# Kernel optimization log

Hardware: AMD Instinct MI355X
Metric: run time of the kernel (lower is better)

## Reference

```python
import jax, jax.numpy as jnp
import numpy as np

L, H, DH = 2, 4, 64
D = H * DH                      # hidden_dim*heads = 256
B = 8                           # graphs per batch
NI_PG, ND_PG = 1024, 512        # inst/data nodes per graph
NI, ND = B * NI_PG, B * ND_PG
NPG = NI_PG + ND_PG
KPOOL = NPG // 2                # SAGPooling ratio=0.5
EC, EI, EO, EK = 65536, 32768, 32768, 8192


def setup_inputs():
    key = jax.random.key(0)
    ks = iter(jax.random.split(key, 64))
    def edges(ns, nd, e):
        k1, k2 = jax.random.split(next(ks))
        return jnp.stack([jax.random.randint(k1, (e,), 0, ns),
                          jax.random.randint(k2, (e,), 0, nd)]).astype(jnp.int32)
    inp = {}
    for g in ('g1', 'g2'):
        inp[g + '_x_inst'] = 0.1 * jax.random.normal(next(ks), (NI, D), jnp.float32)
        inp[g + '_x_data'] = 0.1 * jax.random.normal(next(ks), (ND, D), jnp.float32)
        inp[g + '_e_control'] = edges(NI, NI, EC)
        inp[g + '_e_input'] = edges(ND, NI, EI)
        inp[g + '_e_output'] = edges(NI, ND, EO)
        inp[g + '_e_call'] = edges(NI, NI, EK)
    s = 1.0 / np.sqrt(D)
    def w(*shape):
        return s * jax.random.normal(next(ks), shape, jnp.float32)
    for name in ('hgt_Wk', 'hgt_Wq', 'hgt_Wv', 'hgt_Wo'):
        inp[name] = w(L, 2, 2, D, D)   # [layer, direction, node_type, D, D]
    sh = 1.0 / np.sqrt(DH)
    inp['hgt_arel'] = sh * jax.random.normal(next(ks), (L, 2, 4, H, DH, DH), jnp.float32)
    inp['hgt_mrel'] = sh * jax.random.normal(next(ks), (L, 2, 4, H, DH, DH), jnp.float32)
    inp['hgt_prel'] = jnp.ones((L, 2, 4, H), jnp.float32)
    inp['hgt_skip'] = jnp.ones((L, 2, 2), jnp.float32)
    inp['pool_W'] = w(D, 1)
    inp['pool_att'] = 0.1 * jax.random.normal(next(ks), (2,), jnp.float32)
    inp['pool_bias'] = jnp.zeros((1,), jnp.float32)
    for name in ('trans_Wq', 'trans_Wk', 'trans_Wv', 'trans_Wo'):
        inp[name] = w(D, D)
    inp['trans_ln_g'] = jnp.ones((D,), jnp.float32)
    inp['trans_ln_b'] = jnp.zeros((D,), jnp.float32)
    return inp


def _seg_softmax_agg(scores, vals, col, n):
    # scores [E,H], vals [E,H,DH], softmax over incoming edges per dst node
    m = jax.ops.segment_max(scores, col, num_segments=n)
    a = jnp.exp(scores - m[col])
    den = jax.ops.segment_sum(a, col, num_segments=n)
    alpha = a / (den[col] + 1e-16)
    return jax.ops.segment_sum(alpha[..., None] * vals, col, num_segments=n)


def _hgt_conv(xs, rels, Wk, Wq, Wv, Wo, arel, mrel, prel, skip):
    # xs: [x_inst, x_data]; rels: list of (rel_idx, src_t, dst_t, row, col)
    ns = [x.shape[0] for x in xs]
    K = [(x @ Wk[t]).reshape(-1, H, DH) for t, x in enumerate(xs)]
    Q = [(x @ Wq[t]).reshape(-1, H, DH) for t, x in enumerate(xs)]
    V = [(x @ Wv[t]).reshape(-1, H, DH) for t, x in enumerate(xs)]
    buf = {0: ([], [], []), 1: ([], [], [])}
    for r, st, dt, row, col in rels:
        ke = jnp.einsum('ehd,hdf->ehf', K[st][row], arel[r])
        ve = jnp.einsum('ehd,hdf->ehf', V[st][row], mrel[r])
        sc = (Q[dt][col] * ke).sum(-1) * prel[r] / np.sqrt(DH)   # [E,H]
        buf[dt][0].append(sc); buf[dt][1].append(ve); buf[dt][2].append(col)
    out = []
    for t, x in enumerate(xs):
        sc = jnp.concatenate(buf[t][0])
        ve = jnp.concatenate(buf[t][1])
        col = jnp.concatenate(buf[t][2])
        agg = _seg_softmax_agg(sc, ve, col, ns[t]).reshape(ns[t], D)
        o = jax.nn.gelu(agg, approximate=False) @ Wo[t]
        g = jax.nn.sigmoid(skip[t])
        out.append(g * o + (1.0 - g) * x)
    return out


def _dir_hgt(xs, E, P, l):
    (rc, cc), (ri, ci), (ro, co), (rk, ck) = [(e[0], e[1]) for e in E]
    fwd_rels = [(0, 0, 0, rc, cc), (1, 1, 0, ri, ci), (2, 0, 1, ro, co), (3, 0, 0, rk, ck)]
    rev_rels = [(0, 0, 0, cc, rc), (1, 0, 1, ci, ri), (2, 1, 0, co, ro), (3, 0, 0, ck, rk)]
    of = _hgt_conv(xs, fwd_rels, *[p[l, 0] for p in P])
    orv = _hgt_conv(xs, rev_rels, *[p[l, 1] for p in P])
    return [0.5 * a + 0.5 * b for a, b in zip(of, orv)]   # alpha = 0.5


def _branch(x_i, x_d, ec, ei, eo, ek, P, pool_W, pool_att, pool_bias, tq, tk, tv, to, lg, lb):
    xs = [x_i, x_d]
    E = (ec, ei, eo, ek)
    for l in range(L):
        xs = _dir_hgt(xs, E, P, l)
        xs = [jax.nn.relu(x) for x in xs]        # dropout is identity at eval
    x = jnp.concatenate(xs, 0)                   # to_homogeneous: inst then data
    N = NI + ND
    loops = jnp.arange(N, dtype=jnp.int32)       # GATConv add_self_loops=True
    row = jnp.concatenate([ec[0], ei[0] + NI, eo[0], ek[0], loops])
    col = jnp.concatenate([ec[1], ei[1], eo[1] + NI, ek[1], loops])
    # SAGPooling score via 1-channel GATConv
    h = x @ pool_W                               # [N,1]
    e = jax.nn.leaky_relu(pool_att[0] * h[row, 0] + pool_att[1] * h[col, 0], negative_slope=0.2)
    m = jax.ops.segment_max(e, col, num_segments=N)
    a = jnp.exp(e - m[col])
    den = jax.ops.segment_sum(a, col, num_segments=N)
    score = jax.ops.segment_sum((a / (den[col] + 1e-16)) * h[row, 0], col, num_segments=N) + pool_bias[0]
    # regroup nodes per graph (graphs contiguous within each node type block)
    sg = jnp.concatenate([score[:NI].reshape(B, NI_PG), score[NI:].reshape(B, ND_PG)], 1)
    xg = jnp.concatenate([x[:NI].reshape(B, NI_PG, D), x[NI:].reshape(B, ND_PG, D)], 1)
    vals, idx = jax.lax.top_k(sg, KPOOL)
    xp = jnp.take_along_axis(xg, idx[:, :, None], axis=1) * jnp.tanh(vals)[:, :, None]
    # global transformer attention over pooled nodes of each graph (TransConv)
    q = (xp @ tq).reshape(B, KPOOL, H, DH)
    k_ = (xp @ tk).reshape(B, KPOOL, H, DH)
    v = (xp @ tv).reshape(B, KPOOL, H, DH)
    att = jax.nn.softmax(jnp.einsum('bqhd,bkhd->bhqk', q, k_) / np.sqrt(DH), -1)
    o = jnp.einsum('bhqk,bkhd->bqhd', att, v).reshape(B, KPOOL, D) @ to
    y = xp + o
    mu = y.mean(-1, keepdims=True)
    var = ((y - mu) ** 2).mean(-1, keepdims=True)
    gatt = lg * (y - mu) / jnp.sqrt(var + 1e-5) + lb
    feat = jnp.concatenate([xp, gatt], -1)       # [B, KPOOL, 2D]
    return feat.sum(1)                           # global_add_pool -> [B, 2D]


def reference(g1_x_inst, g1_x_data, g1_e_control, g1_e_input, g1_e_output, g1_e_call,
              g2_x_inst, g2_x_data, g2_e_control, g2_e_input, g2_e_output, g2_e_call,
              hgt_Wk, hgt_Wq, hgt_Wv, hgt_Wo, hgt_arel, hgt_mrel, hgt_prel, hgt_skip,
              pool_W, pool_att, pool_bias,
              trans_Wq, trans_Wk, trans_Wv, trans_Wo, trans_ln_g, trans_ln_b):
    P = (hgt_Wk, hgt_Wq, hgt_Wv, hgt_Wo, hgt_arel, hgt_mrel, hgt_prel, hgt_skip)
    u = _branch(g1_x_inst, g1_x_data, g1_e_control, g1_e_input, g1_e_output, g1_e_call,
                P, pool_W, pool_att, pool_bias, trans_Wq, trans_Wk, trans_Wv, trans_Wo,
                trans_ln_g, trans_ln_b)
    v = _branch(g2_x_inst, g2_x_data, g2_e_control, g2_e_input, g2_e_output, g2_e_call,
                P, pool_W, pool_att, pool_bias, trans_Wq, trans_Wk, trans_Wv, trans_Wo,
                trans_ln_g, trans_ln_b)
    num = (u * v).sum(-1)
    den = jnp.maximum(jnp.linalg.norm(u, axis=-1), 1e-8) * jnp.maximum(jnp.linalg.norm(v, axis=-1), 1e-8)
    return num / den                             # cosine similarity, [B]
```

## Files before the change

### kernel.cpp

```cpp
#include <hip/hip_runtime.h>
#include <math.h>
#include <stdint.h>

#define LL 2
#define HH 4
#define DHH 64
#define DD 256
#define BB 8
#define NI 8192
#define ND 4096
#define NROW 12288
#define KPOOL 768
#define EC 65536
#define EI 32768
#define EO 32768
#define EK 8192
#define EHGT (EC+EI+EO+EK)

typedef unsigned short u16;
typedef short bf16x8 __attribute__((ext_vector_type(8)));
typedef float f32x4 __attribute__((ext_vector_type(4)));
typedef unsigned short u16x4 __attribute__((ext_vector_type(4)));

__device__ inline float gelu_f(float x){ return 0.5f*x*(1.f+erff(x*0.70710678118654752f)); }
__device__ inline u16 f2b(float x){ uint32_t u=__float_as_uint(x); return (u16)((u + 0x7fffu + ((u>>16)&1u))>>16); }
__device__ inline float b2f(u16 h){ return __uint_as_float(((uint32_t)h)<<16); }

__global__ void fill_u32(uint32_t* p, uint32_t v, int n){
    int i = blockIdx.x*256 + threadIdx.x;
    if(i<n) p[i]=v;
}

__global__ void cvt_split(const float* __restrict__ A, int nA, const float* __restrict__ B, int nB,
                          u16* __restrict__ oh, u16* __restrict__ ol){
    int i = (blockIdx.x*256 + threadIdx.x)*4;
    int tot = nA + nB;
    if(i >= tot) return;
    float4 v = (i < nA) ? *(const float4*)(A + i) : *(const float4*)(B + (i - nA));
    float vv[4] = {v.x, v.y, v.z, v.w};
    u16x4 h4, l4;
    #pragma unroll
    for(int j=0;j<4;j++){
        float x = vv[j];
        u16 h = f2b(x);
        h4[j] = h;
        l4[j] = f2b(x - b2f(h));
    }
    *(u16x4*)(oh + i) = h4;
    *(u16x4*)(ol + i) = l4;
}

struct WCArgs { const float* in[8]; u16* oh[8]; u16* ol[8]; int cnt[8]; int nr; };
__global__ void wcvt_split(WCArgs a){
    int mat = blockIdx.y, ri = 0;
    while(ri < a.nr-1 && mat >= a.cnt[ri]){ mat -= a.cnt[ri]; ri++; }
    const float* in = a.in[ri] + (size_t)mat*65536;
    u16* oh = a.oh[ri] + (size_t)mat*65536;
    u16* ol = a.ol[ri] + (size_t)mat*65536;
    int n = blockIdx.x, k = threadIdx.x;
    float x = in[(size_t)k*DD + n];
    u16 h = f2b(x);
    oh[n*DD + k] = h;
    ol[n*DD + k] = f2b(x - b2f(h));
}

struct GDesc { const u16* Ah; const u16* Al; const u16* Bh; const u16* Bl;
               float* C; u16* Oh; u16* Ol;
               const float* X; float* Xacc; const float* skipp;
               int mblks; int mode; int prec; };
struct GArgs { GDesc d[20]; int nd; };

__global__ __launch_bounds__(256) void gemm_mfma(GArgs ga){
    __shared__ u16 SBUF[2*128*64];
    char* Abuf = (char*)SBUF;
    char* Bbuf = (char*)(SBUF + 128*64);
    int mb = blockIdx.x, di = 0;
    while(di < ga.nd-1 && mb >= ga.d[di].mblks){ mb -= ga.d[di].mblks; di++; }
    GDesc g = ga.d[di];
    const int prec = g.prec;
    const int m0 = mb*128, n0 = blockIdx.y*128;
    const int tid = threadIdx.x;
    const int lane = tid & 63, wid = tid >> 6;
    const int wm = (wid>>1)*64, wn = (wid&1)*64;
    const int l15 = lane & 15, l4 = lane >> 4;
    const int srow = tid >> 1, hf = tid & 1;
    const int ssw = (srow&7)<<4;
    const int c0 = (hf*32) ^ ssw;
    const int c1 = (hf*32+16) ^ ssw;
    const int c2 = (64+hf*32) ^ ssw;
    const int c3 = (64+hf*32+16) ^ ssw;
    const int rbyte = srow*128;
    const u16* __restrict__ Aph = g.Ah + (size_t)(m0 + srow)*DD + hf*16;
    const u16* __restrict__ Apl = g.Al + (size_t)(m0 + srow)*DD + hf*16;
    const u16* __restrict__ Bph = g.Bh + (size_t)(n0 + srow)*DD + hf*16;
    const u16* __restrict__ Bpl = g.Bl + (size_t)(n0 + srow)*DD + hf*16;
    f32x4 acc[4][4] = {};
    bf16x8 r0, r1, r2, r3, r4, r5, r6, r7;
    r0 = *(const bf16x8*)(Aph);
    r1 = *(const bf16x8*)(Aph + 8);
    r4 = *(const bf16x8*)(Bph);
    r5 = *(const bf16x8*)(Bph + 8);
    if(!prec){
        r2 = *(const bf16x8*)(Apl);
        r3 = *(const bf16x8*)(Apl + 8);
        r6 = *(const bf16x8*)(Bpl);
        r7 = *(const bf16x8*)(Bpl + 8);
    }
    #pragma unroll
    for(int k0=0;k0<DD;k0+=32){
        __syncthreads();
        *(bf16x8*)(Abuf + rbyte + c0) = r0; *(bf16x8*)(Abuf + rbyte + c1) = r1;
        *(bf16x8*)(Bbuf + rbyte + c0) = r4; *(bf16x8*)(Bbuf + rbyte + c1) = r5;
        if(!prec){
            *(bf16x8*)(Abuf + rbyte + c2) = r2; *(bf16x8*)(Abuf + rbyte + c3) = r3;
            *(bf16x8*)(Bbuf + rbyte + c2) = r6; *(bf16x8*)(Bbuf + rbyte + c3) = r7;
        }
        __syncthreads();
        if(k0 + 32 < DD){
            int kn = k0 + 32;
            r0 = *(const bf16x8*)(Aph + kn);     r1 = *(const bf16x8*)(Aph + kn + 8);
            r4 = *(const bf16x8*)(Bph + kn);     r5 = *(const bf16x8*)(Bph + kn + 8);
            if(!prec){
                r2 = *(const bf16x8*)(Apl + kn); r3 = *(const bf16x8*)(Apl + kn + 8);
                r6 = *(const bf16x8*)(Bpl + kn); r7 = *(const bf16x8*)(Bpl + kn + 8);
            }
        }
        bf16x8 afh[4], bfh[4];
        #pragma unroll
        for(int i=0;i<4;i++){
            int ar = wm + i*16 + l15;
            int abase = ar*128;
            afh[i] = *(const bf16x8*)(Abuf + abase + ((l4*16) ^ ((ar&7)<<4)));
            int br = wn + i*16 + l15;
            int bbase = br*128;
            bfh[i] = *(const bf16x8*)(Bbuf + bbase + ((l4*16) ^ ((br&7)<<4)));
        }
        #pragma unroll
        for(int i=0;i<4;i++)
            #pragma unroll
            for(int j=0;j<4;j++)
                acc[i][j] = __builtin_amdgcn_mfma_f32_16x16x32_bf16(afh[i], bfh[j], acc[i][j], 0,0,0);
        if(!prec){
            bf16x8 afl[4], bfl[4];
            #pragma unroll
            for(int i=0;i<4;i++){
                int ar = wm + i*16 + l15;
                int abase = ar*128;
                afl[i] = *(const bf16x8*)(Abuf + abase + ((64 + l4*16) ^ ((ar&7)<<4)));
                int br = wn + i*16 + l15;
                int bbase = br*128;
                bfl[i] = *(const bf16x8*)(Bbuf + bbase + ((64 + l4*16) ^ ((br&7)<<4)));
            }
            #pragma unroll
            for(int i=0;i<4;i++)
                #pragma unroll
                for(int j=0;j<4;j++){
                    acc[i][j] = __builtin_amdgcn_mfma_f32_16x16x32_bf16(afh[i], bfl[j], acc[i][j], 0,0,0);
                    acc[i][j] = __builtin_amdgcn_mfma_f32_16x16x32_bf16(afl[i], bfh[j], acc[i][j], 0,0,0);
                }
        }
    }
    const int mode = g.mode;
    float gg = 0.f;
    if(mode == 2 || mode == 3) gg = 1.f/(1.f + expf(-*g.skipp));
    float* LDSf = (float*)SBUF;
    const int lrow = tid >> 5;
    const int cc4 = (tid & 31)*4;
    #pragma unroll
    for(int half=0; half<2; half++){
        __syncthreads();
        if((wid>>1) == half){
            #pragma unroll
            for(int i=0;i<4;i++)
                #pragma unroll
                for(int j=0;j<4;j++)
                    #pragma unroll
                    for(int r=0;r<4;r++)
                        LDSf[(i*16 + l4*4 + r)*128 + wn + j*16 + l15] = acc[i][j][r];
        }
        __syncthreads();
        #pragma unroll
        for(int k=0;k<8;k++){
            int row = lrow + k*8;
            size_t o = (size_t)(m0 + half*64 + row)*DD + n0 + cc4;
            float4 v = *(const float4*)&LDSf[row*128 + cc4];
            float vv[4] = {v.x, v.y, v.z, v.w};
            if(mode==0){
                *(float4*)(g.C + o) = v;
            } else if(mode==4){
                u16x4 h4;
                #pragma unroll
                for(int j=0;j<4;j++) h4[j] = f2b(vv[j]);
                *(u16x4*)(g.Oh + o) = h4;
            } else if(mode==1){
                u16x4 h4, lo4;
                #pragma unroll
                for(int j=0;j<4;j++){
                    u16 hh = f2b(vv[j]); h4[j]=hh; lo4[j]=f2b(vv[j]-b2f(hh));
                }
                *(u16x4*)(g.Oh + o) = h4;
                *(u16x4*)(g.Ol + o) = lo4;
            } else if(mode==2){
                float4 x = *(const float4*)(g.X + o);
                float xx[4] = {x.x, x.y, x.z, x.w};
                float4 w;
                float* ww = (float*)&w;
                #pragma unroll
                for(int j=0;j<4;j++) ww[j] = 0.5f*(gg*vv[j] + (1.f-gg)*xx[j]);
                *(float4*)(g.Xacc + o) = w;
            } else {
                float4 x = *(const float4*)(g.X + o);
                float4 xa = *(const float4*)(g.Xacc + o);
                float xx[4] = {x.x, x.y, x.z, x.w};
                float aa[4] = {xa.x, xa.y, xa.z, xa.w};
                float4 cv;
                float* cvv = (float*)&cv;
                u16x4 h4, lo4;
                #pragma unroll
                for(int j=0;j<4;j++){
                    float v3 = aa[j] + 0.5f*(gg*vv[j] + (1.f-gg)*xx[j]);
                    v3 = v3 > 0.f ? v3 : 0.f;
                    cvv[j] = v3;
                    u16 hh = f2b(v3); h4[j]=hh; lo4[j]=f2b(v3-b2f(hh));
                }
                *(float4*)(g.C + o) = cv;
                *(u16x4*)(g.Oh + o) = h4;
                *(u16x4*)(g.Ol + o) = lo4;
            }
        }
    }
}

__global__ void combine_all(const float* __restrict__ Wk, const float* __restrict__ Wv,
                            const float* __restrict__ Ra, const float* __restrict__ Rm,
                            float* __restrict__ wtk, float* __restrict__ wtv){
    const int st_tab[2][4] = {{0,1,0,0},{0,0,1,0}};
    int combo = blockIdx.y;
    int idx = combo >> 1, kv = combo & 1;
    int r = idx & 3, wb = idx >> 2, dir = wb & 1;
    int st = st_tab[dir][r];
    const float* W = (kv ? Wv : Wk) + (size_t)(wb*2 + st)*65536;
    const float* R = (kv ? Rm : Ra) + (size_t)idx*16384;
    float* o = (kv ? wtv : wtk) + (size_t)idx*65536;
    int d = blockIdx.x, c = threadIdx.x;
    int h = c >> 6, f = c & 63;
    const float* Wrow = W + d*DD + h*64;
    const float* Rh = R + h*4096 + f;
    float s = 0.f;
    #pragma unroll 8
    for(int k=0;k<64;k++) s += Wrow[k]*Rh[k*64];
    o[d*DD + c] = s;
}

__device__ inline void edge_decode(int e, int& r, int& el){
    if(e < EC){ r=0; el=e; }
    else if(e < EC+EI){ r=1; el=e-EC; }
    else if(e < EC+EI+EO){ r=2; el=e-(EC+EI); }
    else { r=3; el=e-(EC+EI+EO); }
}

struct CB2 {
    const int* row[8]; const int* col[8];
    int dt[8]; int st[8];
    uint32_t* cnt; uint32_t* rowptr; uint32_t* einfo;
};

__global__ void csr_hist2(CB2 a){
    int ge = blockIdx.x*256 + threadIdx.x;
    if(ge >= 2*EHGT) return;
    int dir = ge >= EHGT;
    int e = ge - dir*EHGT;
    int r, el; edge_decode(e, r, el);
    int idx = dir*4 + r;
    int c = a.col[idx][el];
    int dst = dir*NROW + (a.dt[idx] ? (NI + c) : c);
    atomicAdd(&a.cnt[dst], 1u);
}

__global__ __launch_bounds__(1024) void scan_rowptr2(uint32_t* cnt, uint32_t* rowptr){
    __shared__ uint32_t part[1024];
    int t = threadIdx.x;
    int base = t*24;
    uint32_t lpre[24];
    uint32_t sum = 0;
    #pragma unroll
    for(int i=0;i<24;i++){
        uint32_t c = cnt[base+i];
        lpre[i] = sum; sum += c;
        cnt[base+i] = 0;
    }
    part[t] = sum;
    __syncthreads();
    for(int offs=1; offs<1024; offs<<=1){
        uint32_t v = (t>=offs) ? part[t-offs] : 0u;
        __syncthreads();
        part[t] += v;
        __syncthreads();
    }
    uint32_t pre = (t==0) ? 0u : part[t-1];
    #pragma unroll
    for(int i=0;i<24;i++) rowptr[base+i] = pre + lpre[i];
    if(t==1023) rowptr[2*NROW] = part[1023];
}

__global__ void csr_scatter2(CB2 a){
    int ge = blockIdx.x*256 + threadIdx.x;
    if(ge >= 2*EHGT) return;
    int dir = ge >= EHGT;
    int e = ge - dir*EHGT;
    int r, el; edge_decode(e, r, el);
    int idx = dir*4 + r;
    int c = a.col[idx][el];
    int dst = dir*NROW + (a.dt[idx] ? (NI + c) : c);
    int src = a.row[idx][el];
    uint32_t p = a.rowptr[dst] + atomicAdd(&a.cnt[dst], 1u);
    uint32_t vmidx = (uint32_t)(r*NI + src);
    uint32_t hom = a.st[idx] ? (uint32_t)(NI + src) : (uint32_t)src;
    a.einfo[p] = vmidx | (hom << 16);
}

__global__ __launch_bounds__(256) void hgt_fused(const uint32_t* __restrict__ rowptr,
                                                 const uint32_t* __restrict__ einfo,
                                                 const float* __restrict__ q_i,
                                                 const float* __restrict__ q_d,
                                                 const u16* __restrict__ ka,
                                                 const u16* __restrict__ vm,
                                                 const float* __restrict__ prel,
                                                 u16* __restrict__ bagg_h,
                                                 u16* __restrict__ bagg_l){
    int wv = threadIdx.x >> 6, lane = threadIdx.x & 63;
    int rowi = blockIdx.x*4 + wv;
    uint32_t p0 = rowptr[rowi], p1 = rowptr[rowi+1];
    int h = lane >> 4;
    const float* qrow = (rowi < NI) ? (q_i + (size_t)rowi*DD) : (q_d + (size_t)(rowi-NI)*DD);
    float4 q4 = *(const float4*)(qrow + lane*4);
    float pr0 = prel[0*HH+h]*0.125f, pr1 = prel[1*HH+h]*0.125f;
    float pr2 = prel[2*HH+h]*0.125f, pr3 = prel[3*HH+h]*0.125f;
    float m = -INFINITY, den = 0.f;
    float4 o4 = {0.f,0.f,0.f,0.f};
    for(uint32_t p = p0; p < p1; p++){
        uint32_t vmidx = einfo[p] & 0xffffu;
        int r = vmidx >> 13;
        uint2 kr = *(const uint2*)(ka + (size_t)vmidx*DD + lane*4);
        uint2 vr = *(const uint2*)(vm + (size_t)vmidx*DD + lane*4);
        float k0 = __uint_as_float(kr.x << 16), k1 = __uint_as_float(kr.x & 0xffff0000u);
        float k2 = __uint_as_float(kr.y << 16), k3 = __uint_as_float(kr.y & 0xffff0000u);
        float v0 = __uint_as_float(vr.x << 16), v1 = __uint_as_float(vr.x & 0xffff0000u);
        float v2 = __uint_as_float(vr.y << 16), v3 = __uint_as_float(vr.y & 0xffff0000u);
        float d = q4.x*k0 + q4.y*k1 + q4.z*k2 + q4.w*k3;
        d += __shfl_xor(d, 1); d += __shfl_xor(d, 2);
        d += __shfl_xor(d, 4); d += __shfl_xor(d, 8);
        float pf = (r==0) ? pr0 : (r==1) ? pr1 : (r==2) ? pr2 : pr3;
        float s = d * pf;
        float nm = fmaxf(m, s);
        float sc_ = expf(m - nm);
        float pe = expf(s - nm);
        den = den*sc_ + pe;
        o4.x = o4.x*sc_ + pe*v0;
        o4.y = o4.y*sc_ + pe*v1;
        o4.z = o4.z*sc_ + pe*v2;
        o4.w = o4.w*sc_ + pe*v3;
        m = nm;
    }
    float inv = 1.f/(den + 1e-16f);
    float vals[4] = {o4.x*inv, o4.y*inv, o4.z*inv, o4.w*inv};
    u16x4 h4, l4;
    #pragma unroll
    for(int j=0;j<4;j++){
        float g = gelu_f(vals[j]);
        u16 hh = f2b(g);
        h4[j] = hh;
        l4[j] = f2b(g - b2f(hh));
    }
    size_t ob = (size_t)rowi*DD + lane*4;
    *(u16x4*)(bagg_h + ob) = h4;
    *(u16x4*)(bagg_l + ob) = l4;
}

__global__ void pool_h2(const float* __restrict__ xi, const float* __restrict__ xd,
                        const float* __restrict__ w, float* __restrict__ h){
    int node = blockIdx.x*4 + (threadIdx.x>>6);
    int lane = threadIdx.x & 63;
    const float* xr = (node < NI) ? (xi + (size_t)node*DD) : (xd + (size_t)(node-NI)*DD);
    float s = 0.f;
    for(int j=lane;j<DD;j+=64) s += xr[j]*w[j];
    for(int m=32;m;m>>=1) s += __shfl_xor(s, m);
    if(lane==0) h[node] = s;
}

__global__ __launch_bounds__(256) void pool_csr(const uint32_t* __restrict__ rowptr,
                                                const uint32_t* __restrict__ einfo,
                                                const float* __restrict__ h,
                                                const float* __restrict__ att,
                                                float* __restrict__ score){
    int w = blockIdx.x*4 + (threadIdx.x >> 6);
    int lane = threadIdx.x & 63;
    if(w >= NROW) return;
    uint32_t p0 = rowptr[w], p1 = rowptr[w+1];
    float a0 = att[0], a1 = att[1];
    float hn = h[w];
    float es = a0*hn + a1*hn;
    es = es >= 0.f ? es : 0.2f*es;
    float m = -INFINITY;
    for(uint32_t p = p0+lane; p < p1; p += 64){
        float hs = h[einfo[p] >> 16];
        float e = a0*hs + a1*hn;
        e = e >= 0.f ? e : 0.2f*e;
        m = fmaxf(m, e);
    }
    #pragma unroll
    for(int s=32;s;s>>=1) m = fmaxf(m, __shfl_xor(m, s));
    m = fmaxf(m, es);
    float lden = 0.f, lnum = 0.f;
    for(uint32_t p = p0+lane; p < p1; p += 64){
        float hs = h[einfo[p] >> 16];
        float e = a0*hs + a1*hn;
        e = e >= 0.f ? e : 0.2f*e;
        float a = expf(e - m);
        lden += a; lnum += a*hs;
    }
    #pragma unroll
    for(int s=32;s;s>>=1){ lden += __shfl_xor(lden, s); lnum += __shfl_xor(lnum, s); }
    float aself = expf(es - m);
    lden += aself; lnum += aself*hn;
    if(lane==0) score[w] = lnum/(lden + 1e-16f);
}

__global__ __launch_bounds__(256) void topk_rank(const float* __restrict__ score,
                                                 const float* __restrict__ bias,
                                                 int* __restrict__ sel_node,
                                                 float* __restrict__ sel_scale){
    int b = blockIdx.y;
    int wid = threadIdx.x >> 6, lane = threadIdx.x & 63;
    int i = blockIdx.x*4 + wid;
    int nodei = (i<1024) ? (b*1024 + i) : (NI + b*512 + (i-1024));
    float ki = score[nodei];
    int r = 0;
    #pragma unroll
    for(int s=0;s<24;s++){
        int j = s*64 + lane;
        int nodej = (j<1024) ? (b*1024 + j) : (NI + b*512 + (j-1024));
        float kj = score[nodej];
        r += (kj > ki) || (kj == ki && j < i);
    }
    #pragma unroll
    for(int m=32;m;m>>=1) r += __shfl_xor(r, m);
    if(lane==0 && r < KPOOL){
        sel_node[b*KPOOL + r] = nodei;
        sel_scale[b*KPOOL + r] = tanhf(ki + bias[0]);
    }
}

__global__ void gather_xp(const int* __restrict__ sel, const float* __restrict__ scale,
                          const float* __restrict__ xi, const float* __restrict__ xd,
                          float* __restrict__ xp, u16* __restrict__ bh, u16* __restrict__ bl){
    int i = blockIdx.x*256 + threadIdx.x;
    int rowp = i >> 8, c = i & 255;
    int node = sel[rowp];
    float s = scale[rowp];
    float v = (node < NI) ? xi[(size_t)node*DD + c] : xd[(size_t)(node-NI)*DD + c];
    float x = v*s;
    xp[i] = x;
    u16 hh = f2b(x);
    bh[i] = hh;
    bl[i] = f2b(x - b2f(hh));
}

__global__ __launch_bounds__(256) void attn_mfma(const u16* __restrict__ Qh,
                                                 const u16* __restrict__ Kh,
                                                 const u16* __restrict__ Vh,
                                                 u16* __restrict__ aoh, u16* __restrict__ aol){
    __shared__ u16 KhS[64*64], VtS[64*64];
    char* KhB = (char*)KhS; char* VtB = (char*)VtS;
    int bh = blockIdx.x;
    int b = bh >> 2, h = bh & 3;
    int q0 = blockIdx.y * 64;
    int tid = threadIdx.x;
    int lane = tid & 63;
    int w = tid >> 6;
    int l15 = lane & 15, l4 = lane >> 4;
    size_t qrow = (size_t)(b*KPOOL + q0 + w*16 + l15);
    bf16x8 qh[2];
    #pragma unroll
    for(int c=0;c<2;c++)
        qh[c] = *(const bf16x8*)(Qh + qrow*DD + h*64 + c*32 + l4*8);
    float mreg = -INFINITY, lreg = 0.f;
    f32x4 O[4] = {};
    for(int k0=0;k0<KPOOL;k0+=64){
        __syncthreads();
        {
            int row = tid >> 2, q4 = tid & 3;
            size_t gbase = ((size_t)(b*KPOOL + k0 + row))*DD + h*64 + q4*16;
            bf16x8 k0v = *(const bf16x8*)(Kh + gbase);
            bf16x8 k1v = *(const bf16x8*)(Kh + gbase + 8);
            int sw = (row&7)<<4;
            int colb = q4*32;
            *(bf16x8*)(KhB + row*128 + (colb ^ sw))      = k0v;
            *(bf16x8*)(KhB + row*128 + ((colb+16) ^ sw)) = k1v;
            int row0 = (tid >> 3)*2, dhg = (tid & 7)*8;
            size_t vbase = ((size_t)(b*KPOOL + k0 + row0))*DD + h*64 + dhg;
            bf16x8 va = *(const bf16x8*)(Vh + vbase);
            bf16x8 vb = *(const bf16x8*)(Vh + vbase + DD);
            #pragma unroll
            for(int j=0;j<8;j++){
                int dh = dhg + j;
                uint32_t pk = (uint32_t)(u16)(short)va[j] | ((uint32_t)(u16)(short)vb[j] << 16);
                *(uint32_t*)(VtB + dh*128 + ((row0*2) ^ ((dh&7)<<4))) = pk;
            }
        }
        __syncthreads();
        f32x4 s[4] = {};
        #pragma unroll
        for(int t=0;t<4;t++){
            int arow = t*16 + l15;
            int sw = (arow&7)<<4;
            const char* bh_ = KhB + arow*128;
            bf16x8 kh0 = *(const bf16x8*)(bh_ + ((l4*16) ^ sw));
            bf16x8 kh1 = *(const bf16x8*)(bh_ + ((l4*16 + 64) ^ sw));
            s[t] = __builtin_amdgcn_mfma_f32_16x16x32_bf16(kh0, qh[0], s[t], 0,0,0);
            s[t] = __builtin_amdgcn_mfma_f32_16x16x32_bf16(kh1, qh[1], s[t], 0,0,0);
        }
        float cm = -INFINITY;
        #pragma unroll
        for(int t=0;t<4;t++)
            #pragma unroll
            for(int r=0;r<4;r++){ s[t][r] *= 0.125f; cm = fmaxf(cm, s[t][r]); }
        cm = fmaxf(cm, __shfl_xor(cm,16));
        cm = fmaxf(cm, __shfl_xor(cm,32));
        float nm = fmaxf(mreg, cm);
        float es = expf(mreg - nm);
        float ps = 0.f;
        #pragma unroll
        for(int t=0;t<4;t++)
            #pragma unroll
            for(int r=0;r<4;r++){ float pv = expf(s[t][r] - nm); s[t][r] = pv; ps += pv; }
        ps += __shfl_xor(ps,16);
        ps += __shfl_xor(ps,32);
        lreg = lreg*es + ps;
        mreg = nm;
        #pragma unroll
        for(int d=0;d<4;d++){ O[d][0]*=es; O[d][1]*=es; O[d][2]*=es; O[d][3]*=es; }
        #pragma unroll
        for(int c32=0;c32<2;c32++){
            bf16x8 pb;
            #pragma unroll
            for(int j=0;j<8;j++){
                int srcl = ((((lane>>4)*2 + (j>>2)) & 3) << 4) | l15;
                float v0 = __shfl(s[c32*2+0][j&3], srcl, 64);
                float v1 = __shfl(s[c32*2+1][j&3], srcl, 64);
                float v = (lane < 32) ? v0 : v1;
                pb[j] = (short)f2b(v);
            }
            #pragma unroll
            for(int dhb=0; dhb<4; dhb++){
                int vrow = dhb*16 + l15;
                bf16x8 va = *(const bf16x8*)(VtB + vrow*128 + ((c32*64 + l4*16) ^ ((vrow&7)<<4)));
                O[dhb] = __builtin_amdgcn_mfma_f32_16x16x32_bf16(va, pb, O[dhb], 0,0,0);
            }
        }
    }
    float inv = 1.f/lreg;
    #pragma unroll
    for(int dhb=0;dhb<4;dhb++)
        #pragma unroll
        for(int r=0;r<4;r++){
            float val = O[dhb][r]*inv;
            size_t o = qrow*DD + h*64 + dhb*16 + l4*4 + r;
            u16 hh = f2b(val);
            aoh[o] = hh;
            aol[o] = f2b(val - b2f(hh));
        }
}

__global__ __launch_bounds__(256) void ln_kernel(const float* __restrict__ xp, const float* __restrict__ o2,
                                                 const float* __restrict__ lg, const float* __restrict__ lb,
                                                 float* __restrict__ gatt){
    __shared__ float red[256];
    int r = blockIdx.x, c = threadIdx.x;
    float y = xp[(size_t)r*DD + c] + o2[(size_t)r*DD + c];
    red[c] = y; __syncthreads();
    for(int s=128;s;s>>=1){ if(c<s) red[c] += red[c+s]; __syncthreads(); }
    float mu = red[0]*(1.f/DD);
    __syncthreads();
    float d = y - mu;
    red[c] = d*d; __syncthreads();
    for(int s=128;s;s>>=1){ if(c<s) red[c] += red[c+s]; __syncthreads(); }
    float var = red[0]*(1.f/DD);
    gatt[(size_t)r*DD + c] = lg[c]*d/sqrtf(var+1e-5f) + lb[c];
}

__global__ void feat_reduce2(const float* __restrict__ xp, const float* __restrict__ gatt,
                             float* __restrict__ out){
    int b = blockIdx.x, c = threadIdx.x;
    int j0 = blockIdx.y*64;
    float s1=0.f, s2=0.f;
    for(int j=j0;j<j0+64;j++){
        size_t base = ((size_t)(b*KPOOL + j))*DD + c;
        s1 += xp[base];
        s2 += gatt[base];
    }
    atomicAdd(&out[b*512 + c], s1);
    atomicAdd(&out[b*512 + 256 + c], s2);
}

__global__ void cosine_kernel(const float* __restrict__ u, const float* __restrict__ v,
                              float* __restrict__ out){
    int b = blockIdx.x, t = threadIdx.x;
    float du=0.f, nu=0.f, nv=0.f;
    for(int j=t;j<512;j+=64){
        float a = u[b*512+j], bb = v[b*512+j];
        du += a*bb; nu += a*a; nv += bb*bb;
    }
    for(int m=32;m;m>>=1){
        du += __shfl_xor(du,m); nu += __shfl_xor(nu,m); nv += __shfl_xor(nv,m);
    }
    if(t==0) out[b] = du / (fmaxf(sqrtf(nu),1e-8f)*fmaxf(sqrtf(nv),1e-8f));
}

extern "C" void kernel_launch(void* const* d_in, const int* in_sizes, int n_in,
                              void* d_out, int out_size, void* d_ws, size_t ws_size,
                              hipStream_t stream){
    (void)in_sizes; (void)n_in; (void)out_size; (void)ws_size;
    const float* hgt_Wk   = (const float*)d_in[12];
    const float* hgt_Wq   = (const float*)d_in[13];
    const float* hgt_Wv   = (const float*)d_in[14];
    const float* hgt_Wo   = (const float*)d_in[15];
    const float* hgt_arel = (const float*)d_in[16];
    const float* hgt_mrel = (const float*)d_in[17];
    const float* hgt_prel = (const float*)d_in[18];
    const float* hgt_skip = (const float*)d_in[19];
    const float* pool_W   = (const float*)d_in[20];
    const float* pool_att = (const float*)d_in[21];
    const float* pool_bias= (const float*)d_in[22];
    const float* t_wq     = (const float*)d_in[23];
    const float* t_wk     = (const float*)d_in[24];
    const float* t_wv     = (const float*)d_in[25];
    const float* t_wo     = (const float*)d_in[26];
    const float* ln_g     = (const float*)d_in[27];
    const float* ln_b     = (const float*)d_in[28];
    float* out = (float*)d_out;

    char* base = (char*)d_ws;
    size_t off = 0;
    auto allocb = [&](size_t nbytes)->void*{
        void* p = (void*)(base + off);
        off += ((nbytes + 255) & ~(size_t)255);
        return p;
    };
    const size_t MAT = 65536;
    u16* bwtk_h = (u16*)allocb(16*MAT*2); u16* bwtk_l = (u16*)allocb(16*MAT*2);
    u16* bwtv_h = (u16*)allocb(16*MAT*2); u16* bwtv_l = (u16*)allocb(16*MAT*2);
    u16* bwq_h  = (u16*)allocb(8*MAT*2);  u16* bwq_l  = (u16*)allocb(8*MAT*2);
    u16* bwo_h  = (u16*)allocb(8*MAT*2);  u16* bwo_l  = (u16*)allocb(8*MAT*2);
    u16* btw_h  = (u16*)allocb(4*MAT*2);  u16* btw_l  = (u16*)allocb(4*MAT*2);
    float* ubuf = (float*)allocb(BB*512*4);
    float* vbuf = (float*)allocb(BB*512*4);
    float* xa_i = (float*)allocb((size_t)NI*DD*4);
    float* xa_d = (float*)allocb((size_t)ND*DD*4);
    float* xb_i = (float*)allocb((size_t)NI*DD*4);
    float* xb_d = (float*)allocb((size_t)ND*DD*4);
    uint32_t* ccnt   = (uint32_t*)allocb((size_t)2*NROW*4);
    uint32_t* rowptr = (uint32_t*)allocb((size_t)(2*NROW+1)*4);
    uint32_t* einfo  = (uint32_t*)allocb((size_t)2*EHGT*4);
    size_t region = off;
    float* q_i  = (float*)allocb((size_t)2*NI*DD*4);
    float* q_d  = (float*)allocb((size_t)2*ND*DD*4);
    u16* ka16 = (u16*)allocb((size_t)8*NI*DD*2);
    u16* vm16 = (u16*)allocb((size_t)8*NI*DD*2);
    float* xacc_i= (float*)allocb((size_t)NI*DD*4);
    float* xacc_d= (float*)allocb((size_t)ND*DD*4);
    u16* bcur_h = (u16*)allocb((size_t)NROW*DD*2);
    u16* bcur_l = (u16*)allocb((size_t)NROW*DD*2);
    u16* bagg_h = (u16*)allocb((size_t)NROW*DD*2);
    u16* bagg_l = (u16*)allocb((size_t)NROW*DD*2);
    off = region;
    float* hvec = (float*)allocb(NROW*4);
    float* pscore = (float*)allocb(NROW*4);
    int* seln   = (int*)allocb(BB*KPOOL*4);
    float* sels = (float*)allocb(BB*KPOOL*4);
    float* xp   = (float*)allocb((size_t)BB*KPOOL*DD*4);
    float* o2   = (float*)allocb((size_t)BB*KPOOL*DD*4);
    float* gatt = (float*)allocb((size_t)BB*KPOOL*DD*4);
    u16* bxp_h = (u16*)allocb((size_t)BB*KPOOL*DD*2);
    u16* bxp_l = (u16*)allocb((size_t)BB*KPOOL*DD*2);
    u16* qbh = (u16*)allocb((size_t)BB*KPOOL*DD*2);
    u16* kbh = (u16*)allocb((size_t)BB*KPOOL*DD*2);
    u16* vbh = (u16*)allocb((size_t)BB*KPOOL*DD*2);
    u16* bao_h = (u16*)allocb((size_t)BB*KPOOL*DD*2);
    u16* bao_l = (u16*)allocb((size_t)BB*KPOOL*DD*2);

    const int st_tab[2][4] = {{0,1,0,0},{0,0,1,0}};
    const int dt_tab[2][4] = {{0,0,1,0},{0,1,0,0}};
    const int MR = BB*KPOOL;

    fill_u32<<<(2*BB*512+255)/256,256,0,stream>>>((uint32_t*)ubuf, 0u, 2*BB*512);
    float* wtkF = (float*)ka16;
    float* wtvF = (float*)ka16 + 16*MAT;
    combine_all<<<dim3(256,32),256,0,stream>>>(hgt_Wk, hgt_Wv, hgt_arel, hgt_mrel, wtkF, wtvF);
    WCArgs wc;
    wc.in[0]=wtkF;   wc.oh[0]=bwtk_h; wc.ol[0]=bwtk_l; wc.cnt[0]=16;
    wc.in[1]=wtvF;   wc.oh[1]=bwtv_h; wc.ol[1]=bwtv_l; wc.cnt[1]=16;
    wc.in[2]=hgt_Wq; wc.oh[2]=bwq_h;  wc.ol[2]=bwq_l;  wc.cnt[2]=8;
    wc.in[3]=hgt_Wo; wc.oh[3]=bwo_h;  wc.ol[3]=bwo_l;  wc.cnt[3]=8;
    wc.in[4]=t_wq;   wc.oh[4]=btw_h;          wc.ol[4]=btw_l;          wc.cnt[4]=1;
    wc.in[5]=t_wk;   wc.oh[5]=btw_h+1*MAT;    wc.ol[5]=btw_l+1*MAT;    wc.cnt[5]=1;
    wc.in[6]=t_wv;   wc.oh[6]=btw_h+2*MAT;    wc.ol[6]=btw_l+2*MAT;    wc.cnt[6]=1;
    wc.in[7]=t_wo;   wc.oh[7]=btw_h+3*MAT;    wc.ol[7]=btw_l+3*MAT;    wc.cnt[7]=1;
    wc.nr = 8;
    wcvt_split<<<dim3(256,52),256,0,stream>>>(wc);

    for(int bi=0;bi<2;bi++){
        int ib = bi*6;
        const float* x_inst = (const float*)d_in[ib+0];
        const float* x_data = (const float*)d_in[ib+1];
        const int* ecp = (const int*)d_in[ib+2];
        const int* eip = (const int*)d_in[ib+3];
        const int* eop = (const int*)d_in[ib+4];
        const int* ekp = (const int*)d_in[ib+5];
        const int* rows_f[4] = {ecp, eip, eop, ekp};
        const int* cols_f[4] = {ecp+EC, eip+EI, eop+EO, ekp+EK};

        CB2 cb;
        for(int r=0;r<4;r++){
            cb.row[r]   = rows_f[r]; cb.col[r]   = cols_f[r]; cb.dt[r]   = dt_tab[0][r]; cb.st[r]   = st_tab[0][r];
            cb.row[4+r] = cols_f[r]; cb.col[4+r] = rows_f[r]; cb.dt[4+r] = dt_tab[1][r]; cb.st[4+r] = st_tab[1][r];
        }
        cb.cnt = ccnt; cb.rowptr = rowptr; cb.einfo = einfo;
        fill_u32<<<(2*NROW+255)/256,256,0,stream>>>(ccnt, 0u, 2*NROW);
        csr_hist2<<<(2*EHGT+255)/256,256,0,stream>>>(cb);
        scan_rowptr2<<<1,1024,0,stream>>>(ccnt, rowptr);
        csr_scatter2<<<(2*EHGT+255)/256,256,0,stream>>>(cb);

        const float* cur_i = x_inst;
        const float* cur_d = x_data;
        cvt_split<<<((NROW*DD/4)+255)/256,256,0,stream>>>(cur_i, NI*DD, cur_d, ND*DD, bcur_h, bcur_l);
        for(int l=0;l<LL;l++){
            float* nxt_i = (l==0) ? xa_i : xb_i;
            float* nxt_d = (l==0) ? xa_d : xb_d;

            GArgs g1; int nb1 = 0, ndx = 0;
            auto addg = [&](int srctype, const u16* Bh, const u16* Bl, float* Cm, u16* Om, int M, int mode, int prec){
                GDesc& d = g1.d[ndx];
                size_t ao = srctype ? (size_t)NI*DD : 0;
                d.Ah = bcur_h + ao; d.Al = bcur_l + ao;
                d.Bh = Bh; d.Bl = Bl; d.C = Cm;
                d.Oh = Om; d.Ol = nullptr; d.X = nullptr; d.Xacc = nullptr; d.skipp = nullptr;
                d.mblks = M/128; d.mode = mode; d.prec = prec;
                nb1 += M/128; ndx++;
            };
            for(int dir=0;dir<2;dir++){
                int wb = l*2 + dir;
                addg(0, bwq_h + (size_t)(wb*2+0)*MAT, bwq_l + (size_t)(wb*2+0)*MAT,
                     q_i + (size_t)dir*NI*DD, nullptr, NI, 0, 0);
                addg(1, bwq_h + (size_t)(wb*2+1)*MAT, bwq_l + (size_t)(wb*2+1)*MAT,
                     q_d + (size_t)dir*ND*DD, nullptr, ND, 0, 0);
                for(int r=0;r<4;r++){
                    int st = st_tab[dir][r];
                    addg(st, bwtk_h + (size_t)(wb*4+r)*MAT, bwtk_l + (size_t)(wb*4+r)*MAT,
                         nullptr, ka16 + (size_t)(dir*4 + r)*NI*DD, st ? ND : NI, 4, 1);
                }
                for(int r=0;r<4;r++){
                    int st = st_tab[dir][r];
                    addg(st, bwtv_h + (size_t)(wb*4+r)*MAT, bwtv_l + (size_t)(wb*4+r)*MAT,
                         nullptr, vm16 + (size_t)(dir*4 + r)*NI*DD, st ? ND : NI, 4, 1);
                }
            }
            g1.nd = ndx;
            gemm_mfma<<<dim3(nb1,2),256,0,stream>>>(g1);

            for(int dir=0;dir<2;dir++){
                int wb = l*2 + dir;

                hgt_fused<<<NROW/4,256,0,stream>>>(rowptr + (size_t)dir*NROW, einfo,
                    q_i + (size_t)dir*NI*DD, q_d + (size_t)dir*ND*DD,
                    ka16 + (size_t)dir*4*NI*DD, vm16 + (size_t)dir*4*NI*DD,
                    hgt_prel + (size_t)wb*4*HH, bagg_h, bagg_l);

                GArgs g3; g3.nd = 2;
                for(int t=0;t<2;t++){
                    GDesc& d = g3.d[t];
                    size_t ao = t ? (size_t)NI*DD : 0;
                    d.Ah = bagg_h + ao; d.Al = bagg_l + ao;
                    d.Bh = bwo_h + (size_t)(wb*2+t)*MAT; d.Bl = bwo_l + (size_t)(wb*2+t)*MAT;
                    d.C = t ? nxt_d : nxt_i;
                    d.Oh = bcur_h + ao; d.Ol = bcur_l + ao;
                    d.X = t ? cur_d : cur_i;
                    d.Xacc = t ? xacc_d : xacc_i;
                    d.skipp = hgt_skip + wb*2 + t;
                    d.mblks = (t ? ND : NI)/128;
                    d.mode = dir ? 3 : 2;
                    d.prec = 0;
                }
                gemm_mfma<<<dim3(NI/128 + ND/128,2),256,0,stream>>>(g3);
            }
            cur_i = nxt_i;
            cur_d = nxt_d;
        }

        pool_h2<<<NROW/4,256,0,stream>>>(cur_i, cur_d, pool_W, hvec);
        pool_csr<<<NROW/4,256,0,stream>>>(rowptr, einfo, hvec, pool_att, pscore);
        topk_rank<<<dim3(384,BB),256,0,stream>>>(pscore, pool_bias, seln, sels);
        gather_xp<<<BB*KPOOL,256,0,stream>>>(seln, sels, cur_i, cur_d, xp, bxp_h, bxp_l);

        GArgs g4; g4.nd = 3;
        for(int t=0;t<3;t++){
            GDesc& d = g4.d[t];
            d.Ah=bxp_h; d.Al=bxp_l;
            d.Bh=btw_h + (size_t)t*MAT; d.Bl=btw_l + (size_t)t*MAT;
            d.C = nullptr;
            d.Oh = (t==0)? qbh : (t==1)? kbh : vbh;
            d.Ol = nullptr;
            d.X = nullptr; d.Xacc = nullptr; d.skipp = nullptr;
            d.mblks = MR/128; d.mode = 4; d.prec = 0;
        }
        gemm_mfma<<<dim3(3*(MR/128),2),256,0,stream>>>(g4);
        attn_mfma<<<dim3(BB*HH, KPOOL/64),256,0,stream>>>(qbh, kbh, vbh, bao_h, bao_l);
        GArgs g5; g5.nd = 1;
        {
            GDesc& d = g5.d[0];
            d.Ah=bao_h; d.Al=bao_l;
            d.Bh=btw_h + (size_t)3*MAT; d.Bl=btw_l + (size_t)3*MAT;
            d.C=o2; d.Oh=nullptr; d.Ol=nullptr; d.X=nullptr; d.Xacc=nullptr; d.skipp=nullptr;
            d.mblks=MR/128; d.mode=0; d.prec=0;
        }
        gemm_mfma<<<dim3(MR/128,2),256,0,stream>>>(g5);
        ln_kernel<<<MR,256,0,stream>>>(xp, o2, ln_g, ln_b, gatt);
        feat_reduce2<<<dim3(BB,12),256,0,stream>>>(xp, gatt, bi ? vbuf : ubuf);
    }

    cosine_kernel<<<BB,64,0,stream>>>(ubuf, vbuf, out);
}
```

Before: 951.0 us.

## Merge both HGT directions into one K=512 output GEMM with prescaled weights

Both edge directions of the HGT aggregation now run in one hgt_fused launch that writes a concatenated [row, 512] aggregate. One output-projection GEMM with K=512 then consumes it, using Wo weights prescaled by 0.5*sigmoid(skip) and stacked along K. The skip and residual terms collapse into a single coefficient on X, which removes the Xacc intermediate buffer, one extra GEMM launch and one hgt launch per layer. In exchange, the GEMM K loop is no longer fully unrolled because K is now a runtime value, and the aggregate buffer doubles in size.

```diff
diff --git a/kernel.cpp b/kernel.cpp
--- a/kernel.cpp
+++ b/kernel.cpp
@@ -64,10 +64,27 @@
     ol[n*DD + k] = f2b(x - b2f(h));
 }
 
+__global__ void wcvt_wo(const float* __restrict__ Wo, const float* __restrict__ skip,
+                        u16* __restrict__ oh, u16* __restrict__ ol){
+    int combo = blockIdx.y;
+    int l = combo >> 1, t = combo & 1;
+    int n = blockIdx.x, k = threadIdx.x;
+    #pragma unroll
+    for(int dir=0;dir<2;dir++){
+        int wi = (l*2+dir)*2 + t;
+        float gg = 1.f/(1.f+expf(-skip[wi]));
+        float x = 0.5f*gg*Wo[(size_t)wi*65536 + (size_t)k*DD + n];
+        size_t o = (size_t)combo*131072 + (size_t)n*512 + dir*256 + k;
+        u16 hh = f2b(x);
+        oh[o] = hh;
+        ol[o] = f2b(x - b2f(hh));
+    }
+}
+
 struct GDesc { const u16* Ah; const u16* Al; const u16* Bh; const u16* Bl;
                float* C; u16* Oh; u16* Ol;
-               const float* X; float* Xacc; const float* skipp;
-               int mblks; int mode; int prec; };
+               const float* X; const float* skipp;
+               int mblks; int mode; int prec; int kdim; };
 struct GArgs { GDesc d[20]; int nd; };
 
 __global__ __launch_bounds__(256) void gemm_mfma(GArgs ga){
@@ -78,6 +95,7 @@
     while(di < ga.nd-1 && mb >= ga.d[di].mblks){ mb -= ga.d[di].mblks; di++; }
     GDesc g = ga.d[di];
     const int prec = g.prec;
+    const int KD = g.kdim;
     const int m0 = mb*128, n0 = blockIdx.y*128;
     const int tid = threadIdx.x;
     const int lane = tid & 63, wid = tid >> 6;
@@ -90,10 +108,10 @@
     const int c2 = (64+hf*32) ^ ssw;
     const int c3 = (64+hf*32+16) ^ ssw;
     const int rbyte = srow*128;
-    const u16* __restrict__ Aph = g.Ah + (size_t)(m0 + srow)*DD + hf*16;
-    const u16* __restrict__ Apl = g.Al + (size_t)(m0 + srow)*DD + hf*16;
-    const u16* __restrict__ Bph = g.Bh + (size_t)(n0 + srow)*DD + hf*16;
-    const u16* __restrict__ Bpl = g.Bl + (size_t)(n0 + srow)*DD + hf*16;
+    const u16* __restrict__ Aph = g.Ah + (size_t)(m0 + srow)*KD + hf*16;
+    const u16* __restrict__ Apl = g.Al + (size_t)(m0 + srow)*KD + hf*16;
+    const u16* __restrict__ Bph = g.Bh + (size_t)(n0 + srow)*KD + hf*16;
+    const u16* __restrict__ Bpl = g.Bl + (size_t)(n0 + srow)*KD + hf*16;
     f32x4 acc[4][4] = {};
     bf16x8 r0, r1, r2, r3, r4, r5, r6, r7;
     r0 = *(const bf16x8*)(Aph);
@@ -106,8 +124,7 @@
         r6 = *(const bf16x8*)(Bpl);
         r7 = *(const bf16x8*)(Bpl + 8);
     }
-    #pragma unroll
-    for(int k0=0;k0<DD;k0+=32){
+    for(int k0=0;k0<KD;k0+=32){
         __syncthreads();
         *(bf16x8*)(Abuf + rbyte + c0) = r0; *(bf16x8*)(Abuf + rbyte + c1) = r1;
         *(bf16x8*)(Bbuf + rbyte + c0) = r4; *(bf16x8*)(Bbuf + rbyte + c1) = r5;
@@ -116,7 +133,7 @@
             *(bf16x8*)(Bbuf + rbyte + c2) = r6; *(bf16x8*)(Bbuf + rbyte + c3) = r7;
         }
         __syncthreads();
-        if(k0 + 32 < DD){
+        if(k0 + 32 < KD){
             int kn = k0 + 32;
             r0 = *(const bf16x8*)(Aph + kn);     r1 = *(const bf16x8*)(Aph + kn + 8);
             r4 = *(const bf16x8*)(Bph + kn);     r5 = *(const bf16x8*)(Bph + kn + 8);
@@ -161,8 +178,12 @@
         }
     }
     const int mode = g.mode;
-    float gg = 0.f;
-    if(mode == 2 || mode == 3) gg = 1.f/(1.f + expf(-*g.skipp));
+    float cx = 0.f;
+    if(mode == 6){
+        float g0 = 1.f/(1.f + expf(-g.skipp[0]));
+        float g1 = 1.f/(1.f + expf(-g.skipp[2]));
+        cx = 1.f - 0.5f*(g0 + g1);
+    }
     float* LDSf = (float*)SBUF;
     const int lrow = tid >> 5;
     const int cc4 = (tid & 31)*4;
@@ -192,33 +213,15 @@
                 #pragma unroll
                 for(int j=0;j<4;j++) h4[j] = f2b(vv[j]);
                 *(u16x4*)(g.Oh + o) = h4;
-            } else if(mode==1){
-                u16x4 h4, lo4;
-                #pragma unroll
-                for(int j=0;j<4;j++){
-                    u16 hh = f2b(vv[j]); h4[j]=hh; lo4[j]=f2b(vv[j]-b2f(hh));
-                }
-                *(u16x4*)(g.Oh + o) = h4;
-                *(u16x4*)(g.Ol + o) = lo4;
-            } else if(mode==2){
+            } else {
                 float4 x = *(const float4*)(g.X + o);
                 float xx[4] = {x.x, x.y, x.z, x.w};
-                float4 w;
-                float* ww = (float*)&w;
-                #pragma unroll
-                for(int j=0;j<4;j++) ww[j] = 0.5f*(gg*vv[j] + (1.f-gg)*xx[j]);
-                *(float4*)(g.Xacc + o) = w;
-            } else {
-                float4 x = *(const float4*)(g.X + o);
-                float4 xa = *(const float4*)(g.Xacc + o);
-                float xx[4] = {x.x, x.y, x.z, x.w};
-                float aa[4] = {xa.x, xa.y, xa.z, xa.w};
                 float4 cv;
                 float* cvv = (float*)&cv;
                 u16x4 h4, lo4;
                 #pragma unroll
                 for(int j=0;j<4;j++){
-                    float v3 = aa[j] + 0.5f*(gg*vv[j] + (1.f-gg)*xx[j]);
+                    float v3 = vv[j] + cx*xx[j];
                     v3 = v3 > 0.f ? v3 : 0.f;
                     cvv[j] = v3;
                     u16 hh = f2b(v3); h4[j]=hh; lo4[j]=f2b(v3-b2f(hh));
@@ -329,20 +332,28 @@
                                                  u16* __restrict__ bagg_h,
                                                  u16* __restrict__ bagg_l){
     int wv = threadIdx.x >> 6, lane = threadIdx.x & 63;
-    int rowi = blockIdx.x*4 + wv;
-    uint32_t p0 = rowptr[rowi], p1 = rowptr[rowi+1];
+    int bx = blockIdx.x;
+    int dir = bx >= (NROW/4);
+    bx -= dir*(NROW/4);
+    int rowi = bx*4 + wv;
+    uint32_t p0 = rowptr[(size_t)dir*NROW + rowi], p1 = rowptr[(size_t)dir*NROW + rowi + 1];
     int h = lane >> 4;
-    const float* qrow = (rowi < NI) ? (q_i + (size_t)rowi*DD) : (q_d + (size_t)(rowi-NI)*DD);
+    const float* qi = q_i + (size_t)dir*NI*DD;
+    const float* qd = q_d + (size_t)dir*ND*DD;
+    const u16* kad = ka + (size_t)dir*4*NI*DD;
+    const u16* vmd = vm + (size_t)dir*4*NI*DD;
+    const float* pr = prel + dir*4*HH;
+    const float* qrow = (rowi < NI) ? (qi + (size_t)rowi*DD) : (qd + (size_t)(rowi-NI)*DD);
     float4 q4 = *(const float4*)(qrow + lane*4);
-    float pr0 = prel[0*HH+h]*0.125f, pr1 = prel[1*HH+h]*0.125f;
-    float pr2 = prel[2*HH+h]*0.125f, pr3 = prel[3*HH+h]*0.125f;
+    float pr0 = pr[0*HH+h]*0.125f, pr1 = pr[1*HH+h]*0.125f;
+    float pr2 = pr[2*HH+h]*0.125f, pr3 = pr[3*HH+h]*0.125f;
     float m = -INFINITY, den = 0.f;
     float4 o4 = {0.f,0.f,0.f,0.f};
     for(uint32_t p = p0; p < p1; p++){
         uint32_t vmidx = einfo[p] & 0xffffu;
         int r = vmidx >> 13;
-        uint2 kr = *(const uint2*)(ka + (size_t)vmidx*DD + lane*4);
-        uint2 vr = *(const uint2*)(vm + (size_t)vmidx*DD + lane*4);
+        uint2 kr = *(const uint2*)(kad + (size_t)vmidx*DD + lane*4);
+        uint2 vr = *(const uint2*)(vmd + (size_t)vmidx*DD + lane*4);
         float k0 = __uint_as_float(kr.x << 16), k1 = __uint_as_float(kr.x & 0xffff0000u);
         float k2 = __uint_as_float(kr.y << 16), k3 = __uint_as_float(kr.y & 0xffff0000u);
         float v0 = __uint_as_float(vr.x << 16), v1 = __uint_as_float(vr.x & 0xffff0000u);
@@ -372,7 +383,7 @@
         h4[j] = hh;
         l4[j] = f2b(g - b2f(hh));
     }
-    size_t ob = (size_t)rowi*DD + lane*4;
+    size_t ob = (size_t)rowi*512 + dir*256 + lane*4;
     *(u16x4*)(bagg_h + ob) = h4;
     *(u16x4*)(bagg_l + ob) = l4;
 }
@@ -651,7 +662,7 @@
     u16* bwtk_h = (u16*)allocb(16*MAT*2); u16* bwtk_l = (u16*)allocb(16*MAT*2);
     u16* bwtv_h = (u16*)allocb(16*MAT*2); u16* bwtv_l = (u16*)allocb(16*MAT*2);
     u16* bwq_h  = (u16*)allocb(8*MAT*2);  u16* bwq_l  = (u16*)allocb(8*MAT*2);
-    u16* bwo_h  = (u16*)allocb(8*MAT*2);  u16* bwo_l  = (u16*)allocb(8*MAT*2);
+    u16* bwoc_h = (u16*)allocb(4*131072*2); u16* bwoc_l = (u16*)allocb(4*131072*2);
     u16* btw_h  = (u16*)allocb(4*MAT*2);  u16* btw_l  = (u16*)allocb(4*MAT*2);
     float* ubuf = (float*)allocb(BB*512*4);
     float* vbuf = (float*)allocb(BB*512*4);
@@ -667,12 +678,10 @@
     float* q_d  = (float*)allocb((size_t)2*ND*DD*4);
     u16* ka16 = (u16*)allocb((size_t)8*NI*DD*2);
     u16* vm16 = (u16*)allocb((size_t)8*NI*DD*2);
-    float* xacc_i= (float*)allocb((size_t)NI*DD*4);
-    float* xacc_d= (float*)allocb((size_t)ND*DD*4);
     u16* bcur_h = (u16*)allocb((size_t)NROW*DD*2);
     u16* bcur_l = (u16*)allocb((size_t)NROW*DD*2);
-    u16* bagg_h = (u16*)allocb((size_t)NROW*DD*2);
-    u16* bagg_l = (u16*)allocb((size_t)NROW*DD*2);
+    u16* bagg_h = (u16*)allocb((size_t)NROW*512*2);
+    u16* bagg_l = (u16*)allocb((size_t)NROW*512*2);
     off = region;
     float* hvec = (float*)allocb(NROW*4);
     float* pscore = (float*)allocb(NROW*4);
@@ -701,13 +710,13 @@
     wc.in[0]=wtkF;   wc.oh[0]=bwtk_h; wc.ol[0]=bwtk_l; wc.cnt[0]=16;
     wc.in[1]=wtvF;   wc.oh[1]=bwtv_h; wc.ol[1]=bwtv_l; wc.cnt[1]=16;
     wc.in[2]=hgt_Wq; wc.oh[2]=bwq_h;  wc.ol[2]=bwq_l;  wc.cnt[2]=8;
-    wc.in[3]=hgt_Wo; wc.oh[3]=bwo_h;  wc.ol[3]=bwo_l;  wc.cnt[3]=8;
-    wc.in[4]=t_wq;   wc.oh[4]=btw_h;          wc.ol[4]=btw_l;          wc.cnt[4]=1;
-    wc.in[5]=t_wk;   wc.oh[5]=btw_h+1*MAT;    wc.ol[5]=btw_l+1*MAT;    wc.cnt[5]=1;
-    wc.in[6]=t_wv;   wc.oh[6]=btw_h+2*MAT;    wc.ol[6]=btw_l+2*MAT;    wc.cnt[6]=1;
-    wc.in[7]=t_wo;   wc.oh[7]=btw_h+3*MAT;    wc.ol[7]=btw_l+3*MAT;    wc.cnt[7]=1;
-    wc.nr = 8;
-    wcvt_split<<<dim3(256,52),256,0,stream>>>(wc);
+    wc.in[3]=t_wq;   wc.oh[3]=btw_h;          wc.ol[3]=btw_l;          wc.cnt[3]=1;
+    wc.in[4]=t_wk;   wc.oh[4]=btw_h+1*MAT;    wc.ol[4]=btw_l+1*MAT;    wc.cnt[4]=1;
+    wc.in[5]=t_wv;   wc.oh[5]=btw_h+2*MAT;    wc.ol[5]=btw_l+2*MAT;    wc.cnt[5]=1;
+    wc.in[6]=t_wo;   wc.oh[6]=btw_h+3*MAT;    wc.ol[6]=btw_l+3*MAT;    wc.cnt[6]=1;
+    wc.nr = 7;
+    wcvt_split<<<dim3(256,44),256,0,stream>>>(wc);
+    wcvt_wo<<<dim3(256,4),256,0,stream>>>(hgt_Wo, hgt_skip, bwoc_h, bwoc_l);
 
     for(int bi=0;bi<2;bi++){
         int ib = bi*6;
@@ -744,8 +753,8 @@
                 size_t ao = srctype ? (size_t)NI*DD : 0;
                 d.Ah = bcur_h + ao; d.Al = bcur_l + ao;
                 d.Bh = Bh; d.Bl = Bl; d.C = Cm;
-                d.Oh = Om; d.Ol = nullptr; d.X = nullptr; d.Xacc = nullptr; d.skipp = nullptr;
-                d.mblks = M/128; d.mode = mode; d.prec = prec;
+                d.Oh = Om; d.Ol = nullptr; d.X = nullptr; d.skipp = nullptr;
+                d.mblks = M/128; d.mode = mode; d.prec = prec; d.kdim = 256;
                 nb1 += M/128; ndx++;
             };
             for(int dir=0;dir<2;dir++){
@@ -768,31 +777,26 @@
             g1.nd = ndx;
             gemm_mfma<<<dim3(nb1,2),256,0,stream>>>(g1);
 
-            for(int dir=0;dir<2;dir++){
-                int wb = l*2 + dir;
-
-                hgt_fused<<<NROW/4,256,0,stream>>>(rowptr + (size_t)dir*NROW, einfo,
-                    q_i + (size_t)dir*NI*DD, q_d + (size_t)dir*ND*DD,
-                    ka16 + (size_t)dir*4*NI*DD, vm16 + (size_t)dir*4*NI*DD,
-                    hgt_prel + (size_t)wb*4*HH, bagg_h, bagg_l);
-
-                GArgs g3; g3.nd = 2;
-                for(int t=0;t<2;t++){
-                    GDesc& d = g3.d[t];
-                    size_t ao = t ? (size_t)NI*DD : 0;
-                    d.Ah = bagg_h + ao; d.Al = bagg_l + ao;
-                    d.Bh = bwo_h + (size_t)(wb*2+t)*MAT; d.Bl = bwo_l + (size_t)(wb*2+t)*MAT;
-                    d.C = t ? nxt_d : nxt_i;
-                    d.Oh = bcur_h + ao; d.Ol = bcur_l + ao;
-                    d.X = t ? cur_d : cur_i;
-                    d.Xacc = t ? xacc_d : xacc_i;
-                    d.skipp = hgt_skip + wb*2 + t;
-                    d.mblks = (t ? ND : NI)/128;
-                    d.mode = dir ? 3 : 2;
-                    d.prec = 0;
-                }
-                gemm_mfma<<<dim3(NI/128 + ND/128,2),256,0,stream>>>(g3);
+            hgt_fused<<<2*(NROW/4),256,0,stream>>>(rowptr, einfo,
+                q_i, q_d, ka16, vm16, hgt_prel + (size_t)l*2*4*HH, bagg_h, bagg_l);
+
+            GArgs g3; g3.nd = 2;
+            for(int t=0;t<2;t++){
+                GDesc& d = g3.d[t];
+                d.Ah = bagg_h + (t ? (size_t)NI*512 : 0);
+                d.Al = bagg_l + (t ? (size_t)NI*512 : 0);
+                d.Bh = bwoc_h + (size_t)(l*2+t)*131072;
+                d.Bl = bwoc_l + (size_t)(l*2+t)*131072;
+                d.C = t ? nxt_d : nxt_i;
+                d.Oh = bcur_h + (t ? (size_t)NI*DD : 0);
+                d.Ol = bcur_l + (t ? (size_t)NI*DD : 0);
+                d.X = t ? cur_d : cur_i;
+                d.skipp = hgt_skip + l*4 + t;
+                d.mblks = (t ? ND : NI)/128;
+                d.mode = 6; d.prec = 0; d.kdim = 512;
             }
+            gemm_mfma<<<dim3(NI/128 + ND/128,2),256,0,stream>>>(g3);
+
             cur_i = nxt_i;
             cur_d = nxt_d;
         }
@@ -810,8 +814,8 @@
             d.C = nullptr;
             d.Oh = (t==0)? qbh : (t==1)? kbh : vbh;
             d.Ol = nullptr;
-            d.X = nullptr; d.Xacc = nullptr; d.skipp = nullptr;
-            d.mblks = MR/128; d.mode = 4; d.prec = 0;
+            d.X = nullptr; d.skipp = nullptr;
+            d.mblks = MR/128; d.mode = 4; d.prec = 0; d.kdim = 256;
         }
         gemm_mfma<<<dim3(3*(MR/128),2),256,0,stream>>>(g4);
         attn_mfma<<<dim3(BB*HH, KPOOL/64),256,0,stream>>>(qbh, kbh, vbh, bao_h, bao_l);
@@ -820,8 +824,8 @@
             GDesc& d = g5.d[0];
             d.Ah=bao_h; d.Al=bao_l;
             d.Bh=btw_h + (size_t)3*MAT; d.Bl=btw_l + (size_t)3*MAT;
-            d.C=o2; d.Oh=nullptr; d.Ol=nullptr; d.X=nullptr; d.Xacc=nullptr; d.skipp=nullptr;
-            d.mblks=MR/128; d.mode=0; d.prec=0;
+            d.C=o2; d.Oh=nullptr; d.Ol=nullptr; d.X=nullptr; d.skipp=nullptr;
+            d.mblks=MR/128; d.mode=0; d.prec=0; d.kdim=256;
         }
         gemm_mfma<<<dim3(MR/128,2),256,0,stream>>>(g5);
         ln_kernel<<<MR,256,0,stream>>>(xp, o2, ln_g, ln_b, gatt);
```

New measurement: 917.9 us. 3.5% less time.
